# Kernel optimization log

Hardware: AMD Instinct MI355X
Metric: run time of the kernel (lower is better)

Reference implementation:

```python
import jax, jax.numpy as jnp
import numpy as np

B, D_CAT, C_IN, C_OUT, K, H, W = 16, 512, 256, 256, 3, 64, 64


def setup_inputs() -> dict:
    key = jax.random.key(0)
    ks = jax.random.split(key, 9)
    inp = {
        "x": jax.random.normal(ks[0], (B, C_IN, H, W), dtype=jnp.float32),
        "y": jax.random.normal(ks[1], (B, D_CAT), dtype=jnp.float32),
        # EqualLinear stack: d_catin -> in_channels, then n_dl=2 layers in_channels -> in_channels
        "w0": jax.random.normal(ks[2], (C_IN, D_CAT), dtype=jnp.float32) / np.sqrt(D_CAT),
        "b0": jnp.zeros((C_IN,), dtype=jnp.float32),
        "w1": jax.random.normal(ks[3], (C_IN, C_IN), dtype=jnp.float32) / np.sqrt(C_IN),
        "b1": jnp.zeros((C_IN,), dtype=jnp.float32),
        "w2": jax.random.normal(ks[4], (C_IN, C_IN), dtype=jnp.float32) / np.sqrt(C_IN),
        "b2": jnp.zeros((C_IN,), dtype=jnp.float32),
        # shared conv weight (O, I, k, k), modulated per sample
        "conv_w": jax.random.normal(ks[5], (C_OUT, C_IN, K, K), dtype=jnp.float32) / np.sqrt(C_IN * K * K),
    }
    return inp


def _lrelu(z):
    # nn.LeakyReLU default negative_slope = 0.01
    return jnp.where(z >= 0, z, 0.01 * z)


def reference(x, y, w0, b0, w1, b1, w2, b2, conv_w):
    # style MLP (EqualLinear stack with LeakyReLU)
    s = _lrelu(y @ w0.T + b0)          # (B, C_in)
    s = _lrelu(s @ w1.T + b1)
    s = _lrelu(s @ w2.T + b2)
    # Per-sample weight modulation: conv(x[b], W * s[b, None, :, None, None]).
    # Since the scale is per input channel (no demodulation), this is exactly
    # equivalent to scaling the input channels and running one shared conv —
    # the fused form a custom kernel would use.
    x_mod = x * s[:, :, None, None]    # (B, C_in, H, W)
    out = jax.lax.conv_general_dilated(
        x_mod, conv_w,
        window_strides=(1, 1),
        padding=((1, 1), (1, 1)),
        dimension_numbers=("NCHW", "OIHW", "NCHW"),
    )  # (B, C_out, H, W); conv has bias=False in _DyConv
    return out
```

## Files before the change

### kernel.cpp

```cpp
#include <hip/hip_runtime.h>

typedef short bf16x8 __attribute__((ext_vector_type(8)));
typedef float f32x4 __attribute__((ext_vector_type(4)));
typedef unsigned short ushort8 __attribute__((ext_vector_type(8)));
typedef unsigned short ushort4v __attribute__((ext_vector_type(4)));

#define BATCH 16
#define DCAT 512
#define CIN 256
#define COUT 256
#define HH 64
#define WW 64
#define HP 66
#define WP 66
#define PLANE (HP * WP * 8)

__device__ __forceinline__ unsigned short f2bf(float f) {
  unsigned int u = __float_as_uint(f);
  unsigned int r = (u + 0x7fffu + ((u >> 16) & 1u)) >> 16;
  return (unsigned short)r;
}

template <int IN_DIM>
__global__ void __launch_bounds__(256) mlp_layer(const float* __restrict__ in,
                                                 const float* __restrict__ w,
                                                 const float* __restrict__ bias,
                                                 float* __restrict__ out) {
  int wid = threadIdx.x >> 6, lane = threadIdx.x & 63;
  int oidx = blockIdx.x * 4 + wid;
  int b = oidx >> 8, c = oidx & 255;
  const float* wr = w + (size_t)c * IN_DIM;
  const float* ir = in + (size_t)b * IN_DIM;
  float sum = 0.f;
#pragma unroll
  for (int d0 = 0; d0 < IN_DIM; d0 += 256) {
    f32x4 wv = *(const f32x4*)(wr + d0 + lane * 4);
    f32x4 iv = *(const f32x4*)(ir + d0 + lane * 4);
    sum += wv[0] * iv[0] + wv[1] * iv[1] + wv[2] * iv[2] + wv[3] * iv[3];
  }
#pragma unroll
  for (int off = 32; off; off >>= 1) sum += __shfl_xor(sum, off, 64);
  if (lane == 0) {
    float a = sum + bias[c];
    out[oidx] = a >= 0.f ? a : 0.01f * a;
  }
}

__global__ void __launch_bounds__(256) prep_all(const float* __restrict__ t1,
                                                const float* __restrict__ w2,
                                                const float* __restrict__ b2,
                                                const float* __restrict__ x,
                                                const float* __restrict__ cw,
                                                unsigned short* __restrict__ xpad,
                                                unsigned short* __restrict__ wt) {
  int blk = blockIdx.x;
  int tid = threadIdx.x;

  if (blk >= 1024) {
    int idx = (blk - 1024) * 256 + tid;
    int t = idx / 16384;
    int r = idx - t * 16384;
    int o = r >> 6, i4 = r & 63;
    ushort4v v;
#pragma unroll
    for (int j = 0; j < 4; j++) v[j] = f2bf(cw[(o * 256 + i4 * 4 + j) * 9 + t]);
    *(ushort4v*)(wt + ((size_t)(t * COUT + o)) * CIN + i4 * 4) = v;
    return;
  }

  int h = blk & 1, c8 = (blk >> 1) & 31, b = blk >> 6;
  int wid = tid >> 6, lane = tid & 63;

  float tv = t1[b * CIN + tid];
  float pj[8];
#pragma unroll
  for (int j = 0; j < 8; j++) pj[j] = w2[(size_t)(c8 * 8 + j) * CIN + tid] * tv;

  const float* xb = x + ((size_t)(b * CIN + c8 * 8)) * (HH * WW);
  int gg0 = h * 512 + tid;
  int gg1 = gg0 + 256;
  int hh0 = (gg0 >> 4) + 1, w00 = (gg0 & 15) * 4 + 1;
  int hh1 = (gg1 >> 4) + 1, w01 = (gg1 & 15) * 4 + 1;
  int base0 = (hh0 - 1) * WW + (w00 - 1);
  int base1 = (hh1 - 1) * WW + (w01 - 1);
  f32x4 v0[8], v1[8];
#pragma unroll
  for (int j = 0; j < 8; j++) v0[j] = *(const f32x4*)(xb + j * (HH * WW) + base0);
#pragma unroll
  for (int j = 0; j < 8; j++) v1[j] = *(const f32x4*)(xb + j * (HH * WW) + base1);

#pragma unroll
  for (int off = 32; off; off >>= 1)
#pragma unroll
    for (int j = 0; j < 8; j++) pj[j] += __shfl_xor(pj[j], off, 64);
  __shared__ float red[4][8];
  __shared__ float sv_sh[8];
  if (lane == 0)
#pragma unroll
    for (int j = 0; j < 8; j++) red[wid][j] = pj[j];
  __syncthreads();
  if (tid < 8) {
    float a = red[0][tid] + red[1][tid] + red[2][tid] + red[3][tid] + b2[c8 * 8 + tid];
    sv_sh[tid] = a >= 0.f ? a : 0.01f * a;
  }
  __syncthreads();
  float sv[8];
#pragma unroll
  for (int j = 0; j < 8; j++) sv[j] = sv_sh[j];

  unsigned short* xp = xpad + ((size_t)(b * 32 + c8)) * PLANE;

  if (tid < 130) {
    int i = h * 130 + tid;
    int bh, bw;
    if (i < 66) { bh = 0; bw = i; }
    else if (i < 132) { bh = 65; bw = i - 66; }
    else if (i < 196) { bh = i - 132 + 1; bw = 0; }
    else { bh = i - 196 + 1; bw = 65; }
    ushort8 z = {0, 0, 0, 0, 0, 0, 0, 0};
    *(ushort8*)(xp + (bh * WP + bw) * 8) = z;
  }

  unsigned short* op0 = xp + (hh0 * WP + w00) * 8;
  unsigned short* op1 = xp + (hh1 * WP + w01) * 8;
#pragma unroll
  for (int t2 = 0; t2 < 4; t2++) {
    ushort8 o;
#pragma unroll
    for (int j = 0; j < 8; j++) o[j] = f2bf(v0[j][t2] * sv[j]);
    *(ushort8*)(op0 + t2 * 8) = o;
  }
#pragma unroll
  for (int t2 = 0; t2 < 4; t2++) {
    ushort8 o;
#pragma unroll
    for (int j = 0; j < 8; j++) o[j] = f2bf(v1[j][t2] * sv[j]);
    *(ushort8*)(op1 + t2 * 8) = o;
  }
}

__device__ __forceinline__ void gl2lds16(const void* g, void* l) {
  __builtin_amdgcn_global_load_lds((const __attribute__((address_space(1))) void*)g,
                                   (__attribute__((address_space(3))) void*)l, 16, 0, 0);
}

__global__ void __launch_bounds__(512, 4) gemm_conv(const unsigned short* __restrict__ xpad,
                                                    const unsigned short* __restrict__ wt,
                                                    float* __restrict__ out) {
  __shared__ unsigned short As[128 * 64];
  __shared__ unsigned short Bs[256 * 64];
  int tid = threadIdx.x;
  int wid = tid >> 6, lane = tid & 63;
  int bid = blockIdx.x;
  int m_t = (bid & 7) * 64 + (bid >> 3);
  int m0 = m_t << 7;
  int b = m0 >> 12;
  int h0 = (m0 >> 6) & 63;
  int wm = wid & 1, wn = wid >> 1;

  f32x4 acc[4][4];
#pragma unroll
  for (int mi = 0; mi < 4; mi++)
#pragma unroll
    for (int ni = 0; ni < 4; ni++) acc[mi][ni] = (f32x4){0.f, 0.f, 0.f, 0.f};

  int p = tid >> 3;
  int cs = tid & 7;
  int gsA = cs ^ (p & 7);
  const unsigned short* aL =
      xpad + ((size_t)((b * 32 + gsA) * HP + h0)) * (WP * 8) + p * 8;
  int o_l = tid >> 3;
  const unsigned short* bL = wt + o_l * CIN + (cs ^ (o_l & 7)) * 8;

  char* As_w0 = (char*)As + wid * 1024;
  char* As_w1 = (char*)As + 8192 + wid * 1024;
  char* Bs_w0 = (char*)Bs + wid * 1024;
  char* Bs_w1 = (char*)Bs + 8192 + wid * 1024;
  char* Bs_w2 = (char*)Bs + 16384 + wid * 1024;
  char* Bs_w3 = (char*)Bs + 24576 + wid * 1024;

  int rA = wm * 64 + (lane & 15);
  int rB = wn * 64 + (lane & 15);
  int qa = lane >> 4;
  int offA0 = rA * 128 + ((qa ^ (rA & 7)) * 16);
  int offA1 = rA * 128 + (((qa + 4) ^ (rA & 7)) * 16);
  int offB0 = rB * 128 + ((qa ^ (rB & 7)) * 16);
  int offB1 = rB * 128 + (((qa + 4) ^ (rB & 7)) * 16);

  for (int kh = 0; kh < 3; kh++) {
    for (int kw = 0; kw < 3; kw++) {
      const unsigned short* aT = aL + (kh * WP + kw) * 8;
      const unsigned short* bT = bL + (kh * 3 + kw) * (COUT * CIN);
#pragma unroll
      for (int kc2 = 0; kc2 < 4; kc2++) {
        const unsigned short* aG = aT + kc2 * (8 * PLANE);
        const unsigned short* bG = bT + kc2 * 64;
        gl2lds16(aG, As_w0);
        gl2lds16(aG + WP * 8, As_w1);
        gl2lds16(bG, Bs_w0);
        gl2lds16(bG + 64 * CIN, Bs_w1);
        gl2lds16(bG + 128 * CIN, Bs_w2);
        gl2lds16(bG + 192 * CIN, Bs_w3);
        __syncthreads();
#pragma unroll
        for (int kb = 0; kb < 2; kb++) {
          int oa = kb ? offA1 : offA0;
          int ob = kb ? offB1 : offB0;
          bf16x8 av[4], bv[4];
#pragma unroll
          for (int mi = 0; mi < 4; mi++)
            av[mi] = *(const bf16x8*)((const char*)As + oa + mi * 2048);
#pragma unroll
          for (int ni = 0; ni < 4; ni++)
            bv[ni] = *(const bf16x8*)((const char*)Bs + ob + ni * 2048);
#pragma unroll
          for (int mi = 0; mi < 4; mi++)
#pragma unroll
            for (int ni = 0; ni < 4; ni++)
              acc[mi][ni] = __builtin_amdgcn_mfma_f32_16x16x32_bf16(av[mi], bv[ni],
                                                                    acc[mi][ni], 0, 0, 0);
        }
        __syncthreads();
      }
    }
  }

  int pixbase = m0 & 4095;
  int quad = lane >> 4;
  int col = lane & 15;
#pragma unroll
  for (int mi = 0; mi < 4; mi++) {
    int pm = pixbase + wm * 64 + mi * 16 + quad * 4;
#pragma unroll
    for (int ni = 0; ni < 4; ni++) {
      int on = wn * 64 + ni * 16 + col;
      float* op = out + ((size_t)(b * COUT + on) << 12) + pm;
      *(f32x4*)op = acc[mi][ni];
    }
  }
}

extern "C" void kernel_launch(void* const* d_in, const int* in_sizes, int n_in,
                              void* d_out, int out_size, void* d_ws, size_t ws_size,
                              hipStream_t stream) {
  const float* x = (const float*)d_in[0];
  const float* y = (const float*)d_in[1];
  const float* w0 = (const float*)d_in[2];
  const float* b0 = (const float*)d_in[3];
  const float* w1 = (const float*)d_in[4];
  const float* b1 = (const float*)d_in[5];
  const float* w2 = (const float*)d_in[6];
  const float* b2 = (const float*)d_in[7];
  const float* cw = (const float*)d_in[8];
  float* out = (float*)d_out;

  char* ws = (char*)d_ws;
  float* t0 = (float*)ws;
  float* t1 = (float*)(ws + 16384);
  unsigned short* wt = (unsigned short*)(ws + 32768);
  unsigned short* xpad = (unsigned short*)(ws + 32768 + 9 * COUT * CIN * 2);

  mlp_layer<DCAT><<<BATCH * CIN / 4, 256, 0, stream>>>(y, w0, b0, t0);
  mlp_layer<CIN><<<BATCH * CIN / 4, 256, 0, stream>>>(t0, w1, b1, t1);
  prep_all<<<1024 + 576, 256, 0, stream>>>(t1, w2, b2, x, cw, xpad, wt);
  gemm_conv<<<BATCH * HH * WW / 128, 512, 0, stream>>>(xpad, wt, out);
}
```

Measured before the change: 210.6 us.

## Load conv weights straight to registers and double-buffer activation tiles in LDS

The weight-prep kernel now writes the bf16 conv weights in a pre-swizzled fragment order. Each wave can then read its MFMA B operands directly from global memory into registers, so B no longer goes through LDS. The activation tile is double-buffered in LDS: the next step's tile is prefetched while the current one is consumed, so each K step needs one barrier instead of two. LDS use drops, and the loop is flattened over 36 steps with manual pointer stepping. The cost is that global-load latency for B now sits directly in front of the MFMAs, and two waves load the same B data redundantly.

```diff
diff --git a/kernel.cpp b/kernel.cpp
--- a/kernel.cpp
+++ b/kernel.cpp
@@ -64,7 +64,10 @@
     ushort4v v;
 #pragma unroll
     for (int j = 0; j < 4; j++) v[j] = f2bf(cw[(o * 256 + i4 * 4 + j) * 9 + t]);
-    *(ushort4v*)(wt + ((size_t)(t * COUT + o)) * CIN + i4 * 4) = v;
+    int ob = o >> 4, oo = o & 15;
+    int g4 = i4 >> 3, gr = (i4 >> 1) & 3, j0 = (i4 & 1) * 4;
+    size_t off = ((size_t)((((t * 16 + ob) * 8 + g4) * 4 + gr) * 16 + oo)) * 8 + j0;
+    *(ushort4v*)(wt + off) = v;
     return;
   }
 
@@ -147,8 +150,7 @@
 __global__ void __launch_bounds__(512, 4) gemm_conv(const unsigned short* __restrict__ xpad,
                                                     const unsigned short* __restrict__ wt,
                                                     float* __restrict__ out) {
-  __shared__ unsigned short As[128 * 64];
-  __shared__ unsigned short Bs[256 * 64];
+  __shared__ unsigned short As[2 * 128 * 64];
   int tid = threadIdx.x;
   int wid = tid >> 6, lane = tid & 63;
   int bid = blockIdx.x;
@@ -167,62 +169,65 @@
   int p = tid >> 3;
   int cs = tid & 7;
   int gsA = cs ^ (p & 7);
-  const unsigned short* aL =
+  const unsigned short* aStage =
       xpad + ((size_t)((b * 32 + gsA) * HP + h0)) * (WP * 8) + p * 8;
-  int o_l = tid >> 3;
-  const unsigned short* bL = wt + o_l * CIN + (cs ^ (o_l & 7)) * 8;
-
-  char* As_w0 = (char*)As + wid * 1024;
-  char* As_w1 = (char*)As + 8192 + wid * 1024;
-  char* Bs_w0 = (char*)Bs + wid * 1024;
-  char* Bs_w1 = (char*)Bs + 8192 + wid * 1024;
-  char* Bs_w2 = (char*)Bs + 16384 + wid * 1024;
-  char* Bs_w3 = (char*)Bs + 24576 + wid * 1024;
+
+  int qa = lane >> 4;
+  const char* bp = (const char*)wt + wn * 32768 + qa * 256 + (lane & 15) * 16;
 
   int rA = wm * 64 + (lane & 15);
-  int rB = wn * 64 + (lane & 15);
-  int qa = lane >> 4;
   int offA0 = rA * 128 + ((qa ^ (rA & 7)) * 16);
   int offA1 = rA * 128 + (((qa + 4) ^ (rA & 7)) * 16);
-  int offB0 = rB * 128 + ((qa ^ (rB & 7)) * 16);
-  int offB1 = rB * 128 + (((qa + 4) ^ (rB & 7)) * 16);
-
-  for (int kh = 0; kh < 3; kh++) {
-    for (int kw = 0; kw < 3; kw++) {
-      const unsigned short* aT = aL + (kh * WP + kw) * 8;
-      const unsigned short* bT = bL + (kh * 3 + kw) * (COUT * CIN);
-#pragma unroll
-      for (int kc2 = 0; kc2 < 4; kc2++) {
-        const unsigned short* aG = aT + kc2 * (8 * PLANE);
-        const unsigned short* bG = bT + kc2 * 64;
-        gl2lds16(aG, As_w0);
-        gl2lds16(aG + WP * 8, As_w1);
-        gl2lds16(bG, Bs_w0);
-        gl2lds16(bG + 64 * CIN, Bs_w1);
-        gl2lds16(bG + 128 * CIN, Bs_w2);
-        gl2lds16(bG + 192 * CIN, Bs_w3);
-        __syncthreads();
-#pragma unroll
-        for (int kb = 0; kb < 2; kb++) {
-          int oa = kb ? offA1 : offA0;
-          int ob = kb ? offB1 : offB0;
-          bf16x8 av[4], bv[4];
-#pragma unroll
-          for (int mi = 0; mi < 4; mi++)
-            av[mi] = *(const bf16x8*)((const char*)As + oa + mi * 2048);
-#pragma unroll
-          for (int ni = 0; ni < 4; ni++)
-            bv[ni] = *(const bf16x8*)((const char*)Bs + ob + ni * 2048);
-#pragma unroll
-          for (int mi = 0; mi < 4; mi++)
-#pragma unroll
-            for (int ni = 0; ni < 4; ni++)
-              acc[mi][ni] = __builtin_amdgcn_mfma_f32_16x16x32_bf16(av[mi], bv[ni],
-                                                                    acc[mi][ni], 0, 0, 0);
-        }
-        __syncthreads();
+
+  char* AsB = (char*)As;
+  int stDst = wid * 1024;
+
+  gl2lds16(aStage, AsB + stDst);
+  gl2lds16(aStage + WP * 8, AsB + 8192 + stDst);
+  aStage += 8 * PLANE;
+  __syncthreads();
+
+  int bufoff = 0;
+  for (int s = 0; s < 36; s++) {
+    bf16x8 bv0[4], bv1[4];
+#pragma unroll
+    for (int ni = 0; ni < 4; ni++) {
+      bv0[ni] = *(const bf16x8*)(bp + ni * 8192);
+      bv1[ni] = *(const bf16x8*)(bp + ni * 8192 + 1024);
+    }
+
+    if (s < 35) {
+      char* d = AsB + (bufoff ^ 16384) + stDst;
+      gl2lds16(aStage, d);
+      gl2lds16(aStage + WP * 8, d + 8192);
+      int sn = s + 1;
+      if ((sn & 3) != 3) {
+        aStage += 8 * PLANE;
+      } else {
+        int tapn = sn >> 2;
+        aStage -= 24 * PLANE;
+        aStage += (tapn % 3 != 2) ? 8 : (WP - 2) * 8;
       }
     }
+
+#pragma unroll
+    for (int kb = 0; kb < 2; kb++) {
+      int oa = (kb ? offA1 : offA0) + bufoff;
+      bf16x8 av[4];
+#pragma unroll
+      for (int mi = 0; mi < 4; mi++)
+        av[mi] = *(const bf16x8*)(AsB + oa + mi * 2048);
+#pragma unroll
+      for (int mi = 0; mi < 4; mi++)
+#pragma unroll
+        for (int ni = 0; ni < 4; ni++)
+          acc[mi][ni] = __builtin_amdgcn_mfma_f32_16x16x32_bf16(
+              av[mi], kb ? bv1[ni] : bv0[ni], acc[mi][ni], 0, 0, 0);
+    }
+
+    __syncthreads();
+    bufoff ^= 16384;
+    bp += ((s & 3) != 3) ? 2048 : 124928;
   }
 
   int pixbase = m0 & 4095;
```

Result: slower. 216.5 us (+2.8%).

## Double-buffer LDS and enlarge conv GEMM tile to 256 pixels

Applied to the files above, without the earlier changes.

The implicit-GEMM conv kernel now covers 256 output pixels per block instead of 128, doubling the per-wave accumulator tile to 8x4 MFMA fragments. It uses a 128 KB LDS region with two ping-pong buffers so the next k-slice is loaded asynchronously while the current one is computed, which removes one barrier per step. The grid is halved to 256 blocks and occupancy drops to one block per CU, trading latency hiding by other waves for explicit software pipelining and more reuse of each B tile.

```diff
diff --git a/kernel.cpp b/kernel.cpp
--- a/kernel.cpp
+++ b/kernel.cpp
@@ -144,93 +144,106 @@
                                    (__attribute__((address_space(3))) void*)l, 16, 0, 0);
 }
 
-__global__ void __launch_bounds__(512, 4) gemm_conv(const unsigned short* __restrict__ xpad,
+__global__ void __launch_bounds__(512, 1) gemm_conv(const unsigned short* __restrict__ xpad,
                                                     const unsigned short* __restrict__ wt,
                                                     float* __restrict__ out) {
-  __shared__ unsigned short As[128 * 64];
-  __shared__ unsigned short Bs[256 * 64];
+  __shared__ __align__(16) char lds[131072];
   int tid = threadIdx.x;
   int wid = tid >> 6, lane = tid & 63;
   int bid = blockIdx.x;
-  int m_t = (bid & 7) * 64 + (bid >> 3);
-  int m0 = m_t << 7;
+  int m_t = (bid & 7) * 32 + (bid >> 3);
+  int m0 = m_t << 8;
   int b = m0 >> 12;
   int h0 = (m0 >> 6) & 63;
   int wm = wid & 1, wn = wid >> 1;
 
-  f32x4 acc[4][4];
-#pragma unroll
-  for (int mi = 0; mi < 4; mi++)
+  f32x4 acc[8][4];
+#pragma unroll
+  for (int mi = 0; mi < 8; mi++)
 #pragma unroll
     for (int ni = 0; ni < 4; ni++) acc[mi][ni] = (f32x4){0.f, 0.f, 0.f, 0.f};
 
   int p = tid >> 3;
   int cs = tid & 7;
-  int gsA = cs ^ (p & 7);
-  const unsigned short* aL =
-      xpad + ((size_t)((b * 32 + gsA) * HP + h0)) * (WP * 8) + p * 8;
-  int o_l = tid >> 3;
-  const unsigned short* bL = wt + o_l * CIN + (cs ^ (o_l & 7)) * 8;
-
-  char* As_w0 = (char*)As + wid * 1024;
-  char* As_w1 = (char*)As + 8192 + wid * 1024;
-  char* Bs_w0 = (char*)Bs + wid * 1024;
-  char* Bs_w1 = (char*)Bs + 8192 + wid * 1024;
-  char* Bs_w2 = (char*)Bs + 16384 + wid * 1024;
-  char* Bs_w3 = (char*)Bs + 24576 + wid * 1024;
-
-  int rA = wm * 64 + (lane & 15);
+  int gs = cs ^ (p & 7);
+  const unsigned short* aSt =
+      xpad + ((size_t)((b * 32 + gs) * HP + h0)) * (WP * 8) + p * 8;
+  const unsigned short* bSt = wt + (size_t)p * CIN + gs * 8;
+  int dstOff = wid * 1024;
+
+  int qa = lane >> 4;
+  int rA = wm * 128 + (lane & 15);
   int rB = wn * 64 + (lane & 15);
-  int qa = lane >> 4;
-  int offA0 = rA * 128 + ((qa ^ (rA & 7)) * 16);
-  int offA1 = rA * 128 + (((qa + 4) ^ (rA & 7)) * 16);
-  int offB0 = rB * 128 + ((qa ^ (rB & 7)) * 16);
-  int offB1 = rB * 128 + (((qa + 4) ^ (rB & 7)) * 16);
-
-  for (int kh = 0; kh < 3; kh++) {
-    for (int kw = 0; kw < 3; kw++) {
-      const unsigned short* aT = aL + (kh * WP + kw) * 8;
-      const unsigned short* bT = bL + (kh * 3 + kw) * (COUT * CIN);
-#pragma unroll
-      for (int kc2 = 0; kc2 < 4; kc2++) {
-        const unsigned short* aG = aT + kc2 * (8 * PLANE);
-        const unsigned short* bG = bT + kc2 * 64;
-        gl2lds16(aG, As_w0);
-        gl2lds16(aG + WP * 8, As_w1);
-        gl2lds16(bG, Bs_w0);
-        gl2lds16(bG + 64 * CIN, Bs_w1);
-        gl2lds16(bG + 128 * CIN, Bs_w2);
-        gl2lds16(bG + 192 * CIN, Bs_w3);
-        __syncthreads();
-#pragma unroll
-        for (int kb = 0; kb < 2; kb++) {
-          int oa = kb ? offA1 : offA0;
-          int ob = kb ? offB1 : offB0;
-          bf16x8 av[4], bv[4];
-#pragma unroll
-          for (int mi = 0; mi < 4; mi++)
-            av[mi] = *(const bf16x8*)((const char*)As + oa + mi * 2048);
-#pragma unroll
-          for (int ni = 0; ni < 4; ni++)
-            bv[ni] = *(const bf16x8*)((const char*)Bs + ob + ni * 2048);
-#pragma unroll
-          for (int mi = 0; mi < 4; mi++)
-#pragma unroll
-            for (int ni = 0; ni < 4; ni++)
-              acc[mi][ni] = __builtin_amdgcn_mfma_f32_16x16x32_bf16(av[mi], bv[ni],
-                                                                    acc[mi][ni], 0, 0, 0);
-        }
-        __syncthreads();
+  int offA0 = rA * 128 + ((qa ^ (lane & 7)) * 16);
+  int offA1 = rA * 128 + (((qa + 4) ^ (lane & 7)) * 16);
+  int offB0 = 65536 + rB * 128 + ((qa ^ (lane & 7)) * 16);
+  int offB1 = 65536 + rB * 128 + (((qa + 4) ^ (lane & 7)) * 16);
+
+#define STAGE(bo)                                       \
+  do {                                                  \
+    char* dA = lds + (bo) + dstOff;                     \
+    char* dB = lds + 65536 + (bo) + dstOff;             \
+    gl2lds16(aSt, dA);                                  \
+    gl2lds16(aSt + WP * 8, dA + 8192);                  \
+    gl2lds16(aSt + 2 * WP * 8, dA + 16384);             \
+    gl2lds16(aSt + 3 * WP * 8, dA + 24576);             \
+    gl2lds16(bSt, dB);                                  \
+    gl2lds16(bSt + 64 * CIN, dB + 8192);                \
+    gl2lds16(bSt + 128 * CIN, dB + 16384);              \
+    gl2lds16(bSt + 192 * CIN, dB + 24576);              \
+  } while (0)
+
+  STAGE(0);
+  aSt += 8 * PLANE;
+  bSt += 64;
+  __syncthreads();
+
+  int bo = 0;
+  for (int s = 0; s < 36; s++) {
+    if (s < 35) {
+      STAGE(bo ^ 32768);
+      int sn = s + 1;
+      if ((sn & 3) != 3) {
+        aSt += 8 * PLANE;
+        bSt += 64;
+      } else {
+        int tapn = sn >> 2;
+        aSt += (tapn % 3 != 2) ? (8 - 24 * PLANE) : ((WP - 2) * 8 - 24 * PLANE);
+        bSt += COUT * CIN - 192;
       }
     }
-  }
+
+    const char* Ab = lds + bo;
+#pragma unroll
+    for (int kb = 0; kb < 2; kb++) {
+      int oa = kb ? offA1 : offA0;
+      int ob = kb ? offB1 : offB0;
+      bf16x8 av[8], bv[4];
+#pragma unroll
+      for (int mi = 0; mi < 8; mi++)
+        av[mi] = *(const bf16x8*)(Ab + oa + mi * 2048);
+#pragma unroll
+      for (int ni = 0; ni < 4; ni++)
+        bv[ni] = *(const bf16x8*)(Ab + ob + ni * 2048);
+#pragma unroll
+      for (int mi = 0; mi < 8; mi++)
+#pragma unroll
+        for (int ni = 0; ni < 4; ni++)
+          acc[mi][ni] = __builtin_amdgcn_mfma_f32_16x16x32_bf16(av[mi], bv[ni],
+                                                                acc[mi][ni], 0, 0, 0);
+    }
+
+    __syncthreads();
+    bo ^= 32768;
+  }
+#undef STAGE
 
   int pixbase = m0 & 4095;
   int quad = lane >> 4;
   int col = lane & 15;
 #pragma unroll
-  for (int mi = 0; mi < 4; mi++) {
-    int pm = pixbase + wm * 64 + mi * 16 + quad * 4;
+  for (int mi = 0; mi < 8; mi++) {
+    int pm = pixbase + wm * 128 + mi * 16 + quad * 4;
 #pragma unroll
     for (int ni = 0; ni < 4; ni++) {
       int on = wn * 64 + ni * 16 + col;
@@ -263,5 +276,5 @@
   mlp_layer<DCAT><<<BATCH * CIN / 4, 256, 0, stream>>>(y, w0, b0, t0);
   mlp_layer<CIN><<<BATCH * CIN / 4, 256, 0, stream>>>(t0, w1, b1, t1);
   prep_all<<<1024 + 576, 256, 0, stream>>>(t1, w2, b2, x, cw, xpad, wt);
-  gemm_conv<<<BATCH * HH * WW / 128, 512, 0, stream>>>(xpad, wt, out);
-}
+  gemm_conv<<<BATCH * HH * WW / 256, 512, 0, stream>>>(xpad, wt, out);
+}
```

Result: no change. 209.3 us (-0.6%).

## Fuse style MLP into one kernel and modulate-convert input inside conv GEMM

Applied to the files above, without the earlier changes.

Merges the three style-MLP layers and the weight transpose into a single launch with one block per sample, and drops the padded bf16 copy of x. The conv GEMM now reads fp32 x directly, applies the per-channel style scale and zero padding in registers, converts to bf16 and writes to LDS. This removes two launches and one full write and read of the padded intermediate. In exchange, each GEMM block re-reads fp32 x from global memory once per filter tap with scalar strided loads, and the MLP runs on only 16 blocks.

```diff
diff --git a/kernel.cpp b/kernel.cpp
--- a/kernel.cpp
+++ b/kernel.cpp
@@ -11,9 +11,6 @@
 #define COUT 256
 #define HH 64
 #define WW 64
-#define HP 66
-#define WP 66
-#define PLANE (HP * WP * 8)
 
 __device__ __forceinline__ unsigned short f2bf(float f) {
   unsigned int u = __float_as_uint(f);
@@ -21,43 +18,20 @@
   return (unsigned short)r;
 }
 
-template <int IN_DIM>
-__global__ void __launch_bounds__(256) mlp_layer(const float* __restrict__ in,
-                                                 const float* __restrict__ w,
-                                                 const float* __restrict__ bias,
-                                                 float* __restrict__ out) {
-  int wid = threadIdx.x >> 6, lane = threadIdx.x & 63;
-  int oidx = blockIdx.x * 4 + wid;
-  int b = oidx >> 8, c = oidx & 255;
-  const float* wr = w + (size_t)c * IN_DIM;
-  const float* ir = in + (size_t)b * IN_DIM;
-  float sum = 0.f;
-#pragma unroll
-  for (int d0 = 0; d0 < IN_DIM; d0 += 256) {
-    f32x4 wv = *(const f32x4*)(wr + d0 + lane * 4);
-    f32x4 iv = *(const f32x4*)(ir + d0 + lane * 4);
-    sum += wv[0] * iv[0] + wv[1] * iv[1] + wv[2] * iv[2] + wv[3] * iv[3];
-  }
-#pragma unroll
-  for (int off = 32; off; off >>= 1) sum += __shfl_xor(sum, off, 64);
-  if (lane == 0) {
-    float a = sum + bias[c];
-    out[oidx] = a >= 0.f ? a : 0.01f * a;
-  }
-}
-
-__global__ void __launch_bounds__(256) prep_all(const float* __restrict__ t1,
-                                                const float* __restrict__ w2,
-                                                const float* __restrict__ b2,
-                                                const float* __restrict__ x,
-                                                const float* __restrict__ cw,
-                                                unsigned short* __restrict__ xpad,
-                                                unsigned short* __restrict__ wt) {
-  int blk = blockIdx.x;
-  int tid = threadIdx.x;
-
-  if (blk >= 1024) {
-    int idx = (blk - 1024) * 256 + tid;
+__global__ void __launch_bounds__(1024) mlp_wt(const float* __restrict__ y,
+                                               const float* __restrict__ w0,
+                                               const float* __restrict__ b0,
+                                               const float* __restrict__ w1,
+                                               const float* __restrict__ b1,
+                                               const float* __restrict__ w2,
+                                               const float* __restrict__ b2,
+                                               const float* __restrict__ cw,
+                                               float* __restrict__ sbuf,
+                                               unsigned short* __restrict__ wt) {
+  int tid = threadIdx.x, blk = blockIdx.x;
+
+  if (blk >= 16) {
+    int idx = (blk - 16) * 1024 + tid;
     int t = idx / 16384;
     int r = idx - t * 16384;
     int o = r >> 6, i4 = r & 63;
@@ -68,74 +42,60 @@
     return;
   }
 
-  int h = blk & 1, c8 = (blk >> 1) & 31, b = blk >> 6;
-  int wid = tid >> 6, lane = tid & 63;
-
-  float tv = t1[b * CIN + tid];
-  float pj[8];
-#pragma unroll
-  for (int j = 0; j < 8; j++) pj[j] = w2[(size_t)(c8 * 8 + j) * CIN + tid] * tv;
-
-  const float* xb = x + ((size_t)(b * CIN + c8 * 8)) * (HH * WW);
-  int gg0 = h * 512 + tid;
-  int gg1 = gg0 + 256;
-  int hh0 = (gg0 >> 4) + 1, w00 = (gg0 & 15) * 4 + 1;
-  int hh1 = (gg1 >> 4) + 1, w01 = (gg1 & 15) * 4 + 1;
-  int base0 = (hh0 - 1) * WW + (w00 - 1);
-  int base1 = (hh1 - 1) * WW + (w01 - 1);
-  f32x4 v0[8], v1[8];
-#pragma unroll
-  for (int j = 0; j < 8; j++) v0[j] = *(const f32x4*)(xb + j * (HH * WW) + base0);
-#pragma unroll
-  for (int j = 0; j < 8; j++) v1[j] = *(const f32x4*)(xb + j * (HH * WW) + base1);
-
-#pragma unroll
-  for (int off = 32; off; off >>= 1)
-#pragma unroll
-    for (int j = 0; j < 8; j++) pj[j] += __shfl_xor(pj[j], off, 64);
-  __shared__ float red[4][8];
-  __shared__ float sv_sh[8];
-  if (lane == 0)
-#pragma unroll
-    for (int j = 0; j < 8; j++) red[wid][j] = pj[j];
+  __shared__ float t0s[256], t1s[256];
+  int wv = tid >> 6, lane = tid & 63;
+
+  float yv[8];
+#pragma unroll
+  for (int j = 0; j < 8; j++) yv[j] = y[blk * DCAT + lane * 8 + j];
+  for (int i = 0; i < 16; i++) {
+    int c = wv * 16 + i;
+    const float* wr = w0 + (size_t)c * DCAT + lane * 8;
+    float sum = 0.f;
+#pragma unroll
+    for (int j = 0; j < 8; j++) sum += wr[j] * yv[j];
+#pragma unroll
+    for (int off = 32; off; off >>= 1) sum += __shfl_xor(sum, off, 64);
+    if (lane == 0) {
+      float a = sum + b0[c];
+      t0s[c] = a >= 0.f ? a : 0.01f * a;
+    }
+  }
   __syncthreads();
-  if (tid < 8) {
-    float a = red[0][tid] + red[1][tid] + red[2][tid] + red[3][tid] + b2[c8 * 8 + tid];
-    sv_sh[tid] = a >= 0.f ? a : 0.01f * a;
+
+  float tv[4];
+#pragma unroll
+  for (int j = 0; j < 4; j++) tv[j] = t0s[lane * 4 + j];
+  for (int i = 0; i < 16; i++) {
+    int c = wv * 16 + i;
+    const float* wr = w1 + (size_t)c * CIN + lane * 4;
+    float sum = 0.f;
+#pragma unroll
+    for (int j = 0; j < 4; j++) sum += wr[j] * tv[j];
+#pragma unroll
+    for (int off = 32; off; off >>= 1) sum += __shfl_xor(sum, off, 64);
+    if (lane == 0) {
+      float a = sum + b1[c];
+      t1s[c] = a >= 0.f ? a : 0.01f * a;
+    }
   }
   __syncthreads();
-  float sv[8];
-#pragma unroll
-  for (int j = 0; j < 8; j++) sv[j] = sv_sh[j];
-
-  unsigned short* xp = xpad + ((size_t)(b * 32 + c8)) * PLANE;
-
-  if (tid < 130) {
-    int i = h * 130 + tid;
-    int bh, bw;
-    if (i < 66) { bh = 0; bw = i; }
-    else if (i < 132) { bh = 65; bw = i - 66; }
-    else if (i < 196) { bh = i - 132 + 1; bw = 0; }
-    else { bh = i - 196 + 1; bw = 65; }
-    ushort8 z = {0, 0, 0, 0, 0, 0, 0, 0};
-    *(ushort8*)(xp + (bh * WP + bw) * 8) = z;
-  }
-
-  unsigned short* op0 = xp + (hh0 * WP + w00) * 8;
-  unsigned short* op1 = xp + (hh1 * WP + w01) * 8;
-#pragma unroll
-  for (int t2 = 0; t2 < 4; t2++) {
-    ushort8 o;
-#pragma unroll
-    for (int j = 0; j < 8; j++) o[j] = f2bf(v0[j][t2] * sv[j]);
-    *(ushort8*)(op0 + t2 * 8) = o;
-  }
-#pragma unroll
-  for (int t2 = 0; t2 < 4; t2++) {
-    ushort8 o;
-#pragma unroll
-    for (int j = 0; j < 8; j++) o[j] = f2bf(v1[j][t2] * sv[j]);
-    *(ushort8*)(op1 + t2 * 8) = o;
+
+  float uv[4];
+#pragma unroll
+  for (int j = 0; j < 4; j++) uv[j] = t1s[lane * 4 + j];
+  for (int i = 0; i < 16; i++) {
+    int c = wv * 16 + i;
+    const float* wr = w2 + (size_t)c * CIN + lane * 4;
+    float sum = 0.f;
+#pragma unroll
+    for (int j = 0; j < 4; j++) sum += wr[j] * uv[j];
+#pragma unroll
+    for (int off = 32; off; off >>= 1) sum += __shfl_xor(sum, off, 64);
+    if (lane == 0) {
+      float a = sum + b2[c];
+      sbuf[blk * 256 + c] = a >= 0.f ? a : 0.01f * a;
+    }
   }
 }
 
@@ -144,7 +104,8 @@
                                    (__attribute__((address_space(3))) void*)l, 16, 0, 0);
 }
 
-__global__ void __launch_bounds__(512, 4) gemm_conv(const unsigned short* __restrict__ xpad,
+__global__ void __launch_bounds__(512, 4) gemm_conv(const float* __restrict__ x,
+                                                    const float* __restrict__ sbuf,
                                                     const unsigned short* __restrict__ wt,
                                                     float* __restrict__ out) {
   __shared__ unsigned short As[128 * 64];
@@ -164,16 +125,14 @@
 #pragma unroll
     for (int ni = 0; ni < 4; ni++) acc[mi][ni] = (f32x4){0.f, 0.f, 0.f, 0.f};
 
-  int p = tid >> 3;
-  int cs = tid & 7;
-  int gsA = cs ^ (p & 7);
-  const unsigned short* aL =
-      xpad + ((size_t)((b * 32 + gsA) * HP + h0)) * (WP * 8) + p * 8;
+  int p = lane;
+  char* wA0 = (char*)As + p * 128 + ((wid ^ (p & 7)) * 16);
+  char* wA1 = wA0 + 64 * 128;
+  const float* xb = x + (size_t)b * CIN * (HH * WW);
+
   int o_l = tid >> 3;
-  const unsigned short* bL = wt + o_l * CIN + (cs ^ (o_l & 7)) * 8;
-
-  char* As_w0 = (char*)As + wid * 1024;
-  char* As_w1 = (char*)As + 8192 + wid * 1024;
+  int csb = tid & 7;
+  const unsigned short* bL = wt + o_l * CIN + (csb ^ (o_l & 7)) * 8;
   char* Bs_w0 = (char*)Bs + wid * 1024;
   char* Bs_w1 = (char*)Bs + 8192 + wid * 1024;
   char* Bs_w2 = (char*)Bs + 16384 + wid * 1024;
@@ -187,20 +146,40 @@
   int offB0 = rB * 128 + ((qa ^ (rB & 7)) * 16);
   int offB1 = rB * 128 + (((qa + 4) ^ (rB & 7)) * 16);
 
-  for (int kh = 0; kh < 3; kh++) {
-    for (int kw = 0; kw < 3; kw++) {
-      const unsigned short* aT = aL + (kh * WP + kw) * 8;
-      const unsigned short* bT = bL + (kh * 3 + kw) * (COUT * CIN);
-#pragma unroll
-      for (int kc2 = 0; kc2 < 4; kc2++) {
-        const unsigned short* aG = aT + kc2 * (8 * PLANE);
-        const unsigned short* bG = bT + kc2 * 64;
-        gl2lds16(aG, As_w0);
-        gl2lds16(aG + WP * 8, As_w1);
+  for (int kc2 = 0; kc2 < 4; kc2++) {
+    float s8[8];
+#pragma unroll
+    for (int e = 0; e < 8; e++) s8[e] = sbuf[b * 256 + kc2 * 64 + wid * 8 + e];
+    const float* xc = xb + (size_t)(kc2 * 64 + wid * 8) * (HH * WW);
+
+    for (int kh = 0; kh < 3; kh++) {
+      for (int kw = 0; kw < 3; kw++) {
+        const unsigned short* bG = bL + (kh * 3 + kw) * (COUT * CIN) + kc2 * 64;
         gl2lds16(bG, Bs_w0);
         gl2lds16(bG + 64 * CIN, Bs_w1);
         gl2lds16(bG + 128 * CIN, Bs_w2);
         gl2lds16(bG + 192 * CIN, Bs_w3);
+
+        int sr0 = h0 + kh - 1, sr1 = sr0 + 1, sc = p + kw - 1;
+        bool vr0 = (unsigned)sr0 < 64u, vr1 = (unsigned)sr1 < 64u;
+        bool vcc = (unsigned)sc < 64u;
+        int sra0 = sr0 < 0 ? 0 : (sr0 > 63 ? 63 : sr0);
+        int sra1 = sr1 < 0 ? 0 : (sr1 > 63 ? 63 : sr1);
+        int sca = sc < 0 ? 0 : (sc > 63 ? 63 : sc);
+        const float* a0 = xc + sra0 * WW + sca;
+        const float* a1 = xc + sra1 * WW + sca;
+        bool m0v = vr0 && vcc, m1v = vr1 && vcc;
+        ushort8 o0, o1;
+#pragma unroll
+        for (int e = 0; e < 8; e++) {
+          float v0 = a0[e * (HH * WW)];
+          float v1 = a1[e * (HH * WW)];
+          o0[e] = f2bf((m0v ? v0 : 0.f) * s8[e]);
+          o1[e] = f2bf((m1v ? v1 : 0.f) * s8[e]);
+        }
+        *(ushort8*)wA0 = o0;
+        *(ushort8*)wA1 = o1;
+
         __syncthreads();
 #pragma unroll
         for (int kb = 0; kb < 2; kb++) {
@@ -255,13 +234,9 @@
   float* out = (float*)d_out;
 
   char* ws = (char*)d_ws;
-  float* t0 = (float*)ws;
-  float* t1 = (float*)(ws + 16384);
-  unsigned short* wt = (unsigned short*)(ws + 32768);
-  unsigned short* xpad = (unsigned short*)(ws + 32768 + 9 * COUT * CIN * 2);
-
-  mlp_layer<DCAT><<<BATCH * CIN / 4, 256, 0, stream>>>(y, w0, b0, t0);
-  mlp_layer<CIN><<<BATCH * CIN / 4, 256, 0, stream>>>(t0, w1, b1, t1);
-  prep_all<<<1024 + 576, 256, 0, stream>>>(t1, w2, b2, x, cw, xpad, wt);
-  gemm_conv<<<BATCH * HH * WW / 128, 512, 0, stream>>>(xpad, wt, out);
-}
+  float* sbuf = (float*)ws;
+  unsigned short* wt = (unsigned short*)(ws + 16384);
+
+  mlp_wt<<<160, 1024, 0, stream>>>(y, w0, b0, w1, b1, w2, b2, cw, sbuf, wt);
+  gemm_conv<<<BATCH * HH * WW / 128, 512, 0, stream>>>(x, sbuf, wt, out);
+}
```

Result: slower. 300.8 us (+42.8%).
